# Optimization experiments

Measured on AMD Instinct MI355X. Metric: run time of the kernel, lower is better.

The kernel has to match this reference:

```python
import jax, jax.numpy as jnp
import numpy as np

B = 4096
MAX_ATOMS = 2048  # angles_max_length + 1
EPS = 1e-12


def setup_inputs() -> dict:
    key = jax.random.key(0)
    k1, k2, k3 = jax.random.split(key, 3)
    inp = jax.random.normal(k1, (B, 3 * MAX_ATOMS), dtype=jnp.float32)
    tgt = jax.random.normal(k2, (B, 3 * MAX_ATOMS), dtype=jnp.float32)
    lengths = jax.random.randint(k3, (B,), 1, 2047, dtype=jnp.int32)
    return {"input": inp, "target": tgt, "angles_length": lengths}


def _kabsch_rmsd(inp, tgt, angles_length):
    # [B, 3*N] flat xyz -> [B, N, 3]
    b, three_n = inp.shape
    n_atoms_max = three_n // 3
    x = inp.reshape(b, n_atoms_max, 3)
    y = tgt.reshape(b, n_atoms_max, 3)
    # number of valid atoms per sample = angles_length + 1
    n_valid = (angles_length + 1).astype(x.dtype)  # [B]
    mask = (jnp.arange(n_atoms_max)[None, :] < (angles_length[:, None] + 1))
    mask = mask.astype(x.dtype)[..., None]  # [B, N, 1]
    # masked centroids
    denom = n_valid[:, None, None]
    cx = (x * mask).sum(axis=1, keepdims=True) / denom
    cy = (y * mask).sum(axis=1, keepdims=True) / denom
    xc = (x - cx) * mask
    yc = (y - cy) * mask
    # sum of squared norms of both centered point sets
    ssq = (xc * xc).sum(axis=(1, 2)) + (yc * yc).sum(axis=(1, 2))  # [B]
    # 3x3 cross-covariance per sample
    C = jnp.einsum('bni,bnj->bij', xc, yc)  # [B, 3, 3]
    U, S, Vt = jnp.linalg.svd(C)
    # Kabsch det correction (proper rotation)
    d = jnp.sign(jnp.linalg.det(U) * jnp.linalg.det(Vt))  # [B]
    tr = S[:, 0] + S[:, 1] + d * S[:, 2]
    msd = jnp.maximum(ssq - 2.0 * tr, 0.0) / n_valid
    return jnp.sqrt(msd + EPS)


def reference(input, target, angles_length):
    return _kabsch_rmsd(input, target, angles_length)
```

## Files before the change

### kernel.cpp

```cpp
#include <hip/hip_runtime.h>
#include <math.h>


#define NACC 17

__global__ __launch_bounds__(256) void kabsch_rmsd_kernel(
    const float* __restrict__ X,
    const float* __restrict__ Y,
    const int* __restrict__ L,
    float* __restrict__ OUT)
{
    const int row = blockIdx.x;
    const int tid = threadIdx.x;
    const int n = L[row] + 1;

    const float4* xr = (const float4*)(X + (size_t)row * 6144) + (size_t)tid * 6;
    const float4* yr = (const float4*)(Y + (size_t)row * 6144) + (size_t)tid * 6;

    float4 x4[6], y4[6];
#pragma unroll
    for (int i = 0; i < 6; ++i) x4[i] = xr[i];
#pragma unroll
    for (int i = 0; i < 6; ++i) y4[i] = yr[i];

    float fx[24], fy[24];
#pragma unroll
    for (int i = 0; i < 6; ++i) {
        fx[4 * i + 0] = x4[i].x; fx[4 * i + 1] = x4[i].y;
        fx[4 * i + 2] = x4[i].z; fx[4 * i + 3] = x4[i].w;
        fy[4 * i + 0] = y4[i].x; fy[4 * i + 1] = y4[i].y;
        fy[4 * i + 2] = y4[i].z; fy[4 * i + 3] = y4[i].w;
    }

    float v[NACC];
#pragma unroll
    for (int k = 0; k < NACC; ++k) v[k] = 0.0f;

    const int abase = tid * 8;
#pragma unroll
    for (int a = 0; a < 8; ++a) {
        const float msk = (abase + a < n) ? 1.0f : 0.0f;
        const float x0 = fx[3 * a + 0] * msk;
        const float x1 = fx[3 * a + 1] * msk;
        const float x2 = fx[3 * a + 2] * msk;
        const float y0 = fy[3 * a + 0] * msk;
        const float y1 = fy[3 * a + 1] * msk;
        const float y2 = fy[3 * a + 2] * msk;
        v[0] += x0; v[1] += x1; v[2] += x2;
        v[3] += y0; v[4] += y1; v[5] += y2;
        v[6] += x0 * x0 + x1 * x1 + x2 * x2;
        v[7] += y0 * y0 + y1 * y1 + y2 * y2;
        v[8]  += x0 * y0; v[9]  += x0 * y1; v[10] += x0 * y2;
        v[11] += x1 * y0; v[12] += x1 * y1; v[13] += x1 * y2;
        v[14] += x2 * y0; v[15] += x2 * y1; v[16] += x2 * y2;
    }

#pragma unroll
    for (int k = 0; k < NACC; ++k) {
        float t = v[k];
        t += __shfl_down(t, 32);
        t += __shfl_down(t, 16);
        t += __shfl_down(t, 8);
        t += __shfl_down(t, 4);
        t += __shfl_down(t, 2);
        t += __shfl_down(t, 1);
        v[k] = t;
    }

    __shared__ float red[4][NACC];
    const int wave = tid >> 6;
    const int lane = tid & 63;
    if (lane == 0) {
#pragma unroll
        for (int k = 0; k < NACC; ++k) red[wave][k] = v[k];
    }
    __syncthreads();

    if (tid == 0) {
        double s[NACC];
#pragma unroll
        for (int k = 0; k < NACC; ++k)
            s[k] = (double)red[0][k] + (double)red[1][k] +
                   (double)red[2][k] + (double)red[3][k];

        const double inv_n = 1.0 / (double)n;
        const double sx0 = s[0], sx1 = s[1], sx2 = s[2];
        const double sy0 = s[3], sy1 = s[4], sy2 = s[5];
        const double ssq = s[6] + s[7]
            - (sx0 * sx0 + sx1 * sx1 + sx2 * sx2) * inv_n
            - (sy0 * sy0 + sy1 * sy1 + sy2 * sy2) * inv_n;

        double C[3][3];
        C[0][0] = s[8]  - sx0 * sy0 * inv_n;
        C[0][1] = s[9]  - sx0 * sy1 * inv_n;
        C[0][2] = s[10] - sx0 * sy2 * inv_n;
        C[1][0] = s[11] - sx1 * sy0 * inv_n;
        C[1][1] = s[12] - sx1 * sy1 * inv_n;
        C[1][2] = s[13] - sx1 * sy2 * inv_n;
        C[2][0] = s[14] - sx2 * sy0 * inv_n;
        C[2][1] = s[15] - sx2 * sy1 * inv_n;
        C[2][2] = s[16] - sx2 * sy2 * inv_n;

        const double det =
              C[0][0] * (C[1][1] * C[2][2] - C[1][2] * C[2][1])
            - C[0][1] * (C[1][0] * C[2][2] - C[1][2] * C[2][0])
            + C[0][2] * (C[1][0] * C[2][1] - C[1][1] * C[2][0]);

        double A[3][3];
#pragma unroll
        for (int i = 0; i < 3; ++i)
#pragma unroll
            for (int j = 0; j < 3; ++j)
                A[i][j] = C[0][i] * C[0][j] + C[1][i] * C[1][j] + C[2][i] * C[2][j];

        const double q  = (A[0][0] + A[1][1] + A[2][2]) / 3.0;
        const double p1 = A[0][1] * A[0][1] + A[0][2] * A[0][2] + A[1][2] * A[1][2];
        const double a00 = A[0][0] - q, a11 = A[1][1] - q, a22 = A[2][2] - q;
        const double p2 = a00 * a00 + a11 * a11 + a22 * a22 + 2.0 * p1;
        const double p  = sqrt(p2 / 6.0);

        double e1, e2, e3;
        if (p < 1e-30) {
            e1 = e2 = e3 = q;
        } else {
            const double ip = 1.0 / p;
            const double b00 = a00 * ip, b11 = a11 * ip, b22 = a22 * ip;
            const double b01 = A[0][1] * ip, b02 = A[0][2] * ip, b12 = A[1][2] * ip;
            double r = 0.5 * (b00 * (b11 * b22 - b12 * b12)
                            - b01 * (b01 * b22 - b12 * b02)
                            + b02 * (b01 * b12 - b11 * b02));
            r = fmin(1.0, fmax(-1.0, r));
            const double phi = acos(r) / 3.0;
            e1 = q + 2.0 * p * cos(phi);
            e3 = q + 2.0 * p * cos(phi + 2.0 * M_PI / 3.0);
            e2 = 3.0 * q - e1 - e3;
        }

        const double S0 = sqrt(fmax(e1, 0.0));
        const double S1 = sqrt(fmax(e2, 0.0));
        const double S2 = sqrt(fmax(e3, 0.0));
        const double d  = (det > 0.0) ? 1.0 : ((det < 0.0) ? -1.0 : 0.0);
        const double tr = S0 + S1 + d * S2;

        const double msd = fmax(ssq - 2.0 * tr, 0.0) * inv_n;
        OUT[row] = (float)sqrt(msd + 1e-12);
    }
}

extern "C" void kernel_launch(void* const* d_in, const int* in_sizes, int n_in,
                              void* d_out, int out_size, void* d_ws, size_t ws_size,
                              hipStream_t stream) {
    const float* X = (const float*)d_in[0];
    const float* Y = (const float*)d_in[1];
    const int* L = (const int*)d_in[2];
    float* OUT = (float*)d_out;

    const int rows = in_sizes[2];
    kabsch_rmsd_kernel<<<rows, 256, 0, stream>>>(X, Y, L, OUT);
}
```

Baseline: 214.2 us.

## Split Kabsch into moments kernel and batched per-row eigen-solve kernel

Splits the single kernel into two. The first reduces the 17 moment sums per row and writes them to workspace in a transposed layout. The second runs the double-precision 3x3 eigen solve with one thread per row, instead of leaving one thread per block serialising it while the other 255 wait. Loads change from contiguous float4 chunks per thread to strided 12-byte atom reads, which coalesce across threads, and the occupancy hint is raised to 8 blocks. In exchange it adds a second launch and a workspace round trip.

New measurement: 231.7 us. 1.08x slower.

```diff
diff --git a/kernel.cpp b/kernel.cpp
--- a/kernel.cpp
+++ b/kernel.cpp
@@ -4,55 +4,55 @@
 
 #define NACC 17
 
-__global__ __launch_bounds__(256) void kabsch_rmsd_kernel(
+struct F3 { float x, y, z; };
+
+__global__ __launch_bounds__(256, 8) void kabsch_moments_kernel(
     const float* __restrict__ X,
     const float* __restrict__ Y,
     const int* __restrict__ L,
-    float* __restrict__ OUT)
+    float* __restrict__ WS,
+    int B)
 {
     const int row = blockIdx.x;
     const int tid = threadIdx.x;
     const int n = L[row] + 1;
 
-    const float4* xr = (const float4*)(X + (size_t)row * 6144) + (size_t)tid * 6;
-    const float4* yr = (const float4*)(Y + (size_t)row * 6144) + (size_t)tid * 6;
-
-    float4 x4[6], y4[6];
-#pragma unroll
-    for (int i = 0; i < 6; ++i) x4[i] = xr[i];
-#pragma unroll
-    for (int i = 0; i < 6; ++i) y4[i] = yr[i];
-
-    float fx[24], fy[24];
-#pragma unroll
-    for (int i = 0; i < 6; ++i) {
-        fx[4 * i + 0] = x4[i].x; fx[4 * i + 1] = x4[i].y;
-        fx[4 * i + 2] = x4[i].z; fx[4 * i + 3] = x4[i].w;
-        fy[4 * i + 0] = y4[i].x; fy[4 * i + 1] = y4[i].y;
-        fy[4 * i + 2] = y4[i].z; fy[4 * i + 3] = y4[i].w;
-    }
+    const F3* __restrict__ Xr = (const F3*)(X + (size_t)row * 6144);
+    const F3* __restrict__ Yr = (const F3*)(Y + (size_t)row * 6144);
 
     float v[NACC];
 #pragma unroll
     for (int k = 0; k < NACC; ++k) v[k] = 0.0f;
 
-    const int abase = tid * 8;
 #pragma unroll
-    for (int a = 0; a < 8; ++a) {
-        const float msk = (abase + a < n) ? 1.0f : 0.0f;
-        const float x0 = fx[3 * a + 0] * msk;
-        const float x1 = fx[3 * a + 1] * msk;
-        const float x2 = fx[3 * a + 2] * msk;
-        const float y0 = fy[3 * a + 0] * msk;
-        const float y1 = fy[3 * a + 1] * msk;
-        const float y2 = fy[3 * a + 2] * msk;
-        v[0] += x0; v[1] += x1; v[2] += x2;
-        v[3] += y0; v[4] += y1; v[5] += y2;
-        v[6] += x0 * x0 + x1 * x1 + x2 * x2;
-        v[7] += y0 * y0 + y1 * y1 + y2 * y2;
-        v[8]  += x0 * y0; v[9]  += x0 * y1; v[10] += x0 * y2;
-        v[11] += x1 * y0; v[12] += x1 * y1; v[13] += x1 * y2;
-        v[14] += x2 * y0; v[15] += x2 * y1; v[16] += x2 * y2;
+    for (int batch = 0; batch < 2; ++batch) {
+        F3 xa[4], ya[4];
+        int atom[4];
+#pragma unroll
+        for (int i = 0; i < 4; ++i) {
+            atom[i] = (batch * 4 + i) * 256 + tid;
+            xa[i] = Xr[atom[i]];
+        }
+#pragma unroll
+        for (int i = 0; i < 4; ++i) ya[i] = Yr[atom[i]];
+
+#pragma unroll
+        for (int i = 0; i < 4; ++i) {
+            const float msk = (atom[i] < n) ? 1.0f : 0.0f;
+            const float x0 = xa[i].x * msk;
+            const float x1 = xa[i].y * msk;
+            const float x2 = xa[i].z * msk;
+            const float y0 = ya[i].x * msk;
+            const float y1 = ya[i].y * msk;
+            const float y2 = ya[i].z * msk;
+            v[0] += x0; v[1] += x1; v[2] += x2;
+            v[3] += y0; v[4] += y1; v[5] += y2;
+            v[6] += x0 * x0 + x1 * x1 + x2 * x2;
+            v[7] += y0 * y0 + y1 * y1 + y2 * y2;
+            v[8]  += x0 * y0; v[9]  += x0 * y1; v[10] += x0 * y2;
+            v[11] += x1 * y0; v[12] += x1 * y1; v[13] += x1 * y2;
+            v[14] += x2 * y0; v[15] += x2 * y1; v[16] += x2 * y2;
+        }
     }
 
 #pragma unroll
@@ -76,75 +76,88 @@
     }
     __syncthreads();
 
-    if (tid == 0) {
-        double s[NACC];
+    if (tid < NACC) {
+        const float s = red[0][tid] + red[1][tid] + red[2][tid] + red[3][tid];
+        WS[(size_t)tid * B + row] = s;
+    }
+}
+
+__global__ __launch_bounds__(64) void kabsch_eig_kernel(
+    const float* __restrict__ WS,
+    const int* __restrict__ L,
+    float* __restrict__ OUT,
+    int B)
+{
+    const int row = blockIdx.x * 64 + threadIdx.x;
+    if (row >= B) return;
+    const int n = L[row] + 1;
+
+    double s[NACC];
 #pragma unroll
-        for (int k = 0; k < NACC; ++k)
-            s[k] = (double)red[0][k] + (double)red[1][k] +
-                   (double)red[2][k] + (double)red[3][k];
+    for (int k = 0; k < NACC; ++k)
+        s[k] = (double)WS[(size_t)k * B + row];
 
-        const double inv_n = 1.0 / (double)n;
-        const double sx0 = s[0], sx1 = s[1], sx2 = s[2];
-        const double sy0 = s[3], sy1 = s[4], sy2 = s[5];
-        const double ssq = s[6] + s[7]
-            - (sx0 * sx0 + sx1 * sx1 + sx2 * sx2) * inv_n
-            - (sy0 * sy0 + sy1 * sy1 + sy2 * sy2) * inv_n;
+    const double inv_n = 1.0 / (double)n;
+    const double sx0 = s[0], sx1 = s[1], sx2 = s[2];
+    const double sy0 = s[3], sy1 = s[4], sy2 = s[5];
+    const double ssq = s[6] + s[7]
+        - (sx0 * sx0 + sx1 * sx1 + sx2 * sx2) * inv_n
+        - (sy0 * sy0 + sy1 * sy1 + sy2 * sy2) * inv_n;
 
-        double C[3][3];
-        C[0][0] = s[8]  - sx0 * sy0 * inv_n;
-        C[0][1] = s[9]  - sx0 * sy1 * inv_n;
-        C[0][2] = s[10] - sx0 * sy2 * inv_n;
-        C[1][0] = s[11] - sx1 * sy0 * inv_n;
-        C[1][1] = s[12] - sx1 * sy1 * inv_n;
-        C[1][2] = s[13] - sx1 * sy2 * inv_n;
-        C[2][0] = s[14] - sx2 * sy0 * inv_n;
-        C[2][1] = s[15] - sx2 * sy1 * inv_n;
-        C[2][2] = s[16] - sx2 * sy2 * inv_n;
+    double C[3][3];
+    C[0][0] = s[8]  - sx0 * sy0 * inv_n;
+    C[0][1] = s[9]  - sx0 * sy1 * inv_n;
+    C[0][2] = s[10] - sx0 * sy2 * inv_n;
+    C[1][0] = s[11] - sx1 * sy0 * inv_n;
+    C[1][1] = s[12] - sx1 * sy1 * inv_n;
+    C[1][2] = s[13] - sx1 * sy2 * inv_n;
+    C[2][0] = s[14] - sx2 * sy0 * inv_n;
+    C[2][1] = s[15] - sx2 * sy1 * inv_n;
+    C[2][2] = s[16] - sx2 * sy2 * inv_n;
 
-        const double det =
-              C[0][0] * (C[1][1] * C[2][2] - C[1][2] * C[2][1])
-            - C[0][1] * (C[1][0] * C[2][2] - C[1][2] * C[2][0])
-            + C[0][2] * (C[1][0] * C[2][1] - C[1][1] * C[2][0]);
+    const double det =
+          C[0][0] * (C[1][1] * C[2][2] - C[1][2] * C[2][1])
+        - C[0][1] * (C[1][0] * C[2][2] - C[1][2] * C[2][0])
+        + C[0][2] * (C[1][0] * C[2][1] - C[1][1] * C[2][0]);
 
-        double A[3][3];
+    double A[3][3];
 #pragma unroll
-        for (int i = 0; i < 3; ++i)
+    for (int i = 0; i < 3; ++i)
 #pragma unroll
-            for (int j = 0; j < 3; ++j)
-                A[i][j] = C[0][i] * C[0][j] + C[1][i] * C[1][j] + C[2][i] * C[2][j];
+        for (int j = 0; j < 3; ++j)
+            A[i][j] = C[0][i] * C[0][j] + C[1][i] * C[1][j] + C[2][i] * C[2][j];
 
-        const double q  = (A[0][0] + A[1][1] + A[2][2]) / 3.0;
-        const double p1 = A[0][1] * A[0][1] + A[0][2] * A[0][2] + A[1][2] * A[1][2];
-        const double a00 = A[0][0] - q, a11 = A[1][1] - q, a22 = A[2][2] - q;
-        const double p2 = a00 * a00 + a11 * a11 + a22 * a22 + 2.0 * p1;
-        const double p  = sqrt(p2 / 6.0);
+    const double q  = (A[0][0] + A[1][1] + A[2][2]) / 3.0;
+    const double p1 = A[0][1] * A[0][1] + A[0][2] * A[0][2] + A[1][2] * A[1][2];
+    const double a00 = A[0][0] - q, a11 = A[1][1] - q, a22 = A[2][2] - q;
+    const double p2 = a00 * a00 + a11 * a11 + a22 * a22 + 2.0 * p1;
+    const double p  = sqrt(p2 / 6.0);
 
-        double e1, e2, e3;
-        if (p < 1e-30) {
-            e1 = e2 = e3 = q;
-        } else {
-            const double ip = 1.0 / p;
-            const double b00 = a00 * ip, b11 = a11 * ip, b22 = a22 * ip;
-            const double b01 = A[0][1] * ip, b02 = A[0][2] * ip, b12 = A[1][2] * ip;
-            double r = 0.5 * (b00 * (b11 * b22 - b12 * b12)
-                            - b01 * (b01 * b22 - b12 * b02)
-                            + b02 * (b01 * b12 - b11 * b02));
-            r = fmin(1.0, fmax(-1.0, r));
-            const double phi = acos(r) / 3.0;
-            e1 = q + 2.0 * p * cos(phi);
-            e3 = q + 2.0 * p * cos(phi + 2.0 * M_PI / 3.0);
-            e2 = 3.0 * q - e1 - e3;
-        }
+    double e1, e2, e3;
+    if (p < 1e-30) {
+        e1 = e2 = e3 = q;
+    } else {
+        const double ip = 1.0 / p;
+        const double b00 = a00 * ip, b11 = a11 * ip, b22 = a22 * ip;
+        const double b01 = A[0][1] * ip, b02 = A[0][2] * ip, b12 = A[1][2] * ip;
+        double r = 0.5 * (b00 * (b11 * b22 - b12 * b12)
+                        - b01 * (b01 * b22 - b12 * b02)
+                        + b02 * (b01 * b12 - b11 * b02));
+        r = fmin(1.0, fmax(-1.0, r));
+        const double phi = acos(r) / 3.0;
+        e1 = q + 2.0 * p * cos(phi);
+        e3 = q + 2.0 * p * cos(phi + 2.0 * M_PI / 3.0);
+        e2 = 3.0 * q - e1 - e3;
+    }
 
-        const double S0 = sqrt(fmax(e1, 0.0));
-        const double S1 = sqrt(fmax(e2, 0.0));
-        const double S2 = sqrt(fmax(e3, 0.0));
-        const double d  = (det > 0.0) ? 1.0 : ((det < 0.0) ? -1.0 : 0.0);
-        const double tr = S0 + S1 + d * S2;
+    const double S0 = sqrt(fmax(e1, 0.0));
+    const double S1 = sqrt(fmax(e2, 0.0));
+    const double S2 = sqrt(fmax(e3, 0.0));
+    const double d  = (det > 0.0) ? 1.0 : ((det < 0.0) ? -1.0 : 0.0);
+    const double tr = S0 + S1 + d * S2;
 
-        const double msd = fmax(ssq - 2.0 * tr, 0.0) * inv_n;
-        OUT[row] = (float)sqrt(msd + 1e-12);
-    }
+    const double msd = fmax(ssq - 2.0 * tr, 0.0) * inv_n;
+    OUT[row] = (float)sqrt(msd + 1e-12);
 }
 
 extern "C" void kernel_launch(void* const* d_in, const int* in_sizes, int n_in,
@@ -154,7 +167,9 @@
     const float* Y = (const float*)d_in[1];
     const int* L = (const int*)d_in[2];
     float* OUT = (float*)d_out;
+    float* WS = (float*)d_ws;
 
-    const int rows = in_sizes[2];
-    kabsch_rmsd_kernel<<<rows, 256, 0, stream>>>(X, Y, L, OUT);
+    const int B = in_sizes[2];
+    kabsch_moments_kernel<<<B, 256, 0, stream>>>(X, Y, L, WS, B);
+    kabsch_eig_kernel<<<(B + 63) / 64, 64, 0, stream>>>(WS, L, OUT, B);
 }
```
